# Performance work log

Measured on AMD Instinct MI355X. Metric: run time of the kernel, lower is better.

Reference implementation:

```python
import jax, jax.numpy as jnp
import numpy as np

N_NODES = 100000
N_EDGES = 3200000
EMB = 64
K = 2
NUM_GRAPHS = 512


def setup_inputs() -> dict:
    key = jax.random.key(0)
    ks = jax.random.split(key, 12)
    x = jax.random.normal(ks[0], (N_NODES, EMB), dtype=jnp.float32)
    edge_index = jax.random.randint(ks[1], (2, N_EDGES), 0, N_NODES, dtype=jnp.int64)
    edge_attr = jax.random.normal(ks[2], (N_EDGES, 1), dtype=jnp.float32)
    batch = jnp.sort(jax.random.randint(ks[3], (N_NODES,), 0, NUM_GRAPHS, dtype=jnp.int64))
    s = 1.0 / np.sqrt(EMB)
    wn1 = jax.random.normal(ks[4], (EMB, EMB), dtype=jnp.float32) * s
    bn1 = jnp.zeros((EMB,), jnp.float32)
    wn2 = jax.random.normal(ks[5], (EMB, 1), dtype=jnp.float32) * s
    bn2 = jnp.zeros((1,), jnp.float32)
    wc1 = jax.random.normal(ks[6], (EMB, EMB), dtype=jnp.float32) * s
    bc1 = jnp.zeros((EMB,), jnp.float32)
    wc2 = jax.random.normal(ks[7], (EMB, 2 * K * EMB), dtype=jnp.float32) * s
    bc2 = jnp.zeros((2 * K * EMB,), jnp.float32)
    return dict(x=x, edge_index=edge_index, edge_attr=edge_attr, batch=batch,
                wn1=wn1, bn1=bn1, wn2=wn2, bn2=bn2,
                wc1=wc1, bc1=bc1, wc2=wc2, bc2=bc2)


def reference(x, edge_index, edge_attr, batch, wn1, bn1, wn2, bn2, wc1, bc1, wc2, bc2):
    N, C = x.shape
    alpha = 0.1  # APPNP teleport prob
    # --- APPNP(K=1): gcn_norm with self-loops, one propagation step ---
    loops = jnp.arange(N, dtype=edge_index.dtype)
    src = jnp.concatenate([edge_index[0], loops])
    dst = jnp.concatenate([edge_index[1], loops])
    ones = jnp.ones(src.shape[0], dtype=x.dtype)
    deg = jax.ops.segment_sum(ones, dst, num_segments=N)
    dinv = jnp.where(deg > 0, jax.lax.rsqrt(deg), 0.0)
    norm = dinv[src] * dinv[dst]  # [E+N]
    agg = jax.ops.segment_sum(x[src] * norm[:, None], dst, num_segments=N)
    diffuse_x = (1.0 - alpha) * agg + alpha * x  # [N, C]
    # --- node-wise gate: MLP -> global softmax over all nodes ---
    h = jax.nn.relu(diffuse_x @ wn1 + bn1)
    gamma = h @ wn2 + bn2  # [N, 1]
    gamma = jax.nn.softmax(gamma, axis=0)
    # --- per-graph mean pool + channel-wise MLP ---
    sums = jax.ops.segment_sum(diffuse_x, batch, num_segments=NUM_GRAPHS)
    cnt = jax.ops.segment_sum(jnp.ones((N,), x.dtype), batch, num_segments=NUM_GRAPHS)
    pooled = jnp.where(cnt[:, None] > 0, sums / jnp.maximum(cnt, 1.0)[:, None], 0.0)
    pc = jnp.tanh(jax.nn.relu(pooled @ wc1 + bc1) @ wc2 + bc2)  # [B, 2*K*C]
    alpha_kc = pc[:, : K * C].reshape(NUM_GRAPHS, K, C)
    beta_kc = alpha_kc  # faithful to original bug: beta_kc = alpha_kc.reshape(...)
    # --- per-node affine via kron(alpha_kc, gamma_dense) gathered back to nodes ---
    # alpha_batch[b, n, k, c] = alpha_kc[b, k, c] * gamma_dense[b, n]; mask-gather == index by batch
    g = gamma[:, :, None]  # [N, 1, 1]
    a_node = alpha_kc[batch] * g  # [N, K, C]
    b_node = beta_kc[batch] * g  # [N, K, C]
    out = jnp.max(a_node * x[:, None, :] + b_node, axis=1)  # [N, C]
    return out
```

## Files before the change

### kernel.cpp

```cpp
#include <hip/hip_runtime.h>
#include <cstdint>

#define N_NODES   100000
#define N_EDGES   3200000
#define EMB       64
#define NUM_GRAPHS 512
#define NB        391
#define CAP       9216
#define PCHUNK    4096
#define PBLOCKS   ((N_EDGES + PCHUNK - 1) / PCHUNK)

__device__ __forceinline__ float bflo(unsigned u) { return __uint_as_float(u << 16); }
__device__ __forceinline__ float bfhi(unsigned u) { return __uint_as_float(u & 0xFFFF0000u); }
__device__ __forceinline__ unsigned rne_bf16(float f) {
    unsigned b = __float_as_uint(f);
    return (b + 0x7FFFu + ((b >> 16) & 1u)) >> 16;
}

__global__ void cvt_kernel(const float* __restrict__ x, unsigned* __restrict__ xh) {
    int i = blockIdx.x * 256 + threadIdx.x;
    if (i < N_NODES * EMB / 2) {
        float2 f = ((const float2*)x)[i];
        xh[i] = rne_bf16(f.x) | (rne_bf16(f.y) << 16);
    }
}

__global__ void partition_kernel(const int* __restrict__ ei, int* __restrict__ bcnt,
                                 unsigned* __restrict__ gpairs) {
    __shared__ unsigned sp[PCHUNK];
    __shared__ unsigned short sb[PCHUNK];
    __shared__ int scnt[512];
    __shared__ int soff[512];
    __shared__ int scur[512];
    __shared__ int gbase[512];
    __shared__ int s[256];
    int t = threadIdx.x;
    for (int i = t; i < 512; i += 256) scnt[i] = 0;
    __syncthreads();
    int base = blockIdx.x * PCHUNK;
    int lim  = min(N_EDGES - base, PCHUNK);
    for (int k = t; k < lim; k += 256) {
        int d = ei[N_EDGES + base + k];
        atomicAdd(&scnt[d >> 8], 1);
    }
    __syncthreads();
    int a0 = scnt[2 * t], a1 = scnt[2 * t + 1];
    int p = a0 + a1;
    s[t] = p; __syncthreads();
    for (int d = 1; d < 256; d <<= 1) {
        int add = (t >= d) ? s[t - d] : 0;
        __syncthreads();
        s[t] += add;
        __syncthreads();
    }
    int excl = s[t] - p;
    soff[2 * t] = excl;       soff[2 * t + 1] = excl + a0;
    scur[2 * t] = excl;       scur[2 * t + 1] = excl + a0;
    __syncthreads();
    for (int i = t; i < NB; i += 256) gbase[i] = i * CAP + atomicAdd(&bcnt[i], scnt[i]);
    __syncthreads();
    for (int k = t; k < lim; k += 256) {
        int sId = ei[base + k];
        int d   = ei[N_EDGES + base + k];
        int b   = d >> 8;
        int pos = atomicAdd(&scur[b], 1);
        sp[pos] = (unsigned)sId | ((unsigned)(d & 255) << 17);
        sb[pos] = (unsigned short)b;
    }
    __syncthreads();
    for (int i = t; i < lim; i += 256) {
        int b = sb[i];
        gpairs[gbase[b] + (i - soff[b])] = sp[i];
    }
}

__global__ void bucket_scan_kernel(const int* __restrict__ bcnt, int* __restrict__ bbase) {
    __shared__ int s[512];
    int t = threadIdx.x;
    int v = (t < NB) ? bcnt[t] : 0;
    s[t] = v; __syncthreads();
    for (int d = 1; d < 512; d <<= 1) {
        int add = (t >= d) ? s[t - d] : 0;
        __syncthreads();
        s[t] += add;
        __syncthreads();
    }
    if (t < NB) bbase[t] = s[t] - v;
}

__global__ void bscatter2_kernel(const unsigned* __restrict__ gpairs, const int* __restrict__ bcnt,
                                 const int* __restrict__ bbase, int* __restrict__ ebuf,
                                 int* __restrict__ indeg, int* __restrict__ rowstart,
                                 float* __restrict__ dinv) {
    int b = blockIdx.x, t = threadIdx.x, nlo = b << 8;
    __shared__ int lcnt[256];
    __shared__ int lcur[256];
    __shared__ int s[256];
    lcnt[t] = 0; __syncthreads();
    int cnt = bcnt[b];
    const unsigned* gp = gpairs + (size_t)b * CAP;
    for (int i = t; i < cnt; i += 256) atomicAdd(&lcnt[(gp[i] >> 17) & 255], 1);
    __syncthreads();
    int v = lcnt[t];
    s[t] = v; __syncthreads();
    for (int d = 1; d < 256; d <<= 1) {
        int add = (t >= d) ? s[t - d] : 0;
        __syncthreads();
        s[t] += add;
        __syncthreads();
    }
    int excl = s[t] - v;
    int base = bbase[b];
    int n = nlo + t;
    if (n < N_NODES) {
        indeg[n] = v;
        rowstart[n] = base + excl;
        dinv[n] = rsqrtf((float)(v + 1));
    }
    lcur[t] = base + excl;
    __syncthreads();
    for (int i = t; i < cnt; i += 256) {
        unsigned pk = gp[i];
        int pos = atomicAdd(&lcur[(pk >> 17) & 255], 1);
        ebuf[pos] = (int)(pk & 0x1FFFFu);
    }
}

__global__ void gather_mlp_bf16(const int* __restrict__ ebuf, const int* __restrict__ rowstart,
                                const int* __restrict__ indeg, const float* __restrict__ dinv,
                                const float* __restrict__ x, const unsigned* __restrict__ xh,
                                float* __restrict__ dx,
                                const float* __restrict__ wn1, const float* __restrict__ bn1,
                                const float* __restrict__ wn2, const float* __restrict__ bn2,
                                float* __restrict__ gl) {
    __shared__ float wn1s[EMB * EMB];
    __shared__ float bn1s[EMB];
    __shared__ float wn2s[EMB];
    for (int i = threadIdx.x; i < EMB * EMB; i += blockDim.x) wn1s[i] = wn1[i];
    if (threadIdx.x < EMB) { bn1s[threadIdx.x] = bn1[threadIdx.x]; wn2s[threadIdx.x] = wn2[threadIdx.x]; }
    __syncthreads();

    int wid = (blockIdx.x * blockDim.x + threadIdx.x) >> 6;
    if (wid >= N_NODES) return;
    int n = __builtin_amdgcn_readfirstlane(wid);
    int l = threadIdx.x & 63;
    int g = l >> 3;
    int q = l & 7;
    int start = rowstart[n];
    int cnt   = indeg[n];
    float dn  = dinv[n];
    const uint4* __restrict__ xr = (const uint4*)xh;

    float a0 = 0.f, a1 = 0.f, a2 = 0.f, a3 = 0.f, a4 = 0.f, a5 = 0.f, a6 = 0.f, a7 = 0.f;
    int j = 0;
    for (; j + 32 <= cnt; j += 32) {
        int sA = ebuf[start + j + g];
        int sB = ebuf[start + j + 8 + g];
        int sC = ebuf[start + j + 16 + g];
        int sD = ebuf[start + j + 24 + g];
        float wA = dinv[sA] * dn;
        float wB = dinv[sB] * dn;
        float wC = dinv[sC] * dn;
        float wD = dinv[sD] * dn;
        uint4 vA = xr[sA * 8 + q];
        uint4 vB = xr[sB * 8 + q];
        uint4 vC = xr[sC * 8 + q];
        uint4 vD = xr[sD * 8 + q];
        a0 += bflo(vA.x) * wA + bflo(vB.x) * wB + bflo(vC.x) * wC + bflo(vD.x) * wD;
        a1 += bfhi(vA.x) * wA + bfhi(vB.x) * wB + bfhi(vC.x) * wC + bfhi(vD.x) * wD;
        a2 += bflo(vA.y) * wA + bflo(vB.y) * wB + bflo(vC.y) * wC + bflo(vD.y) * wD;
        a3 += bfhi(vA.y) * wA + bfhi(vB.y) * wB + bfhi(vC.y) * wC + bfhi(vD.y) * wD;
        a4 += bflo(vA.z) * wA + bflo(vB.z) * wB + bflo(vC.z) * wC + bflo(vD.z) * wD;
        a5 += bfhi(vA.z) * wA + bfhi(vB.z) * wB + bfhi(vC.z) * wC + bfhi(vD.z) * wD;
        a6 += bflo(vA.w) * wA + bflo(vB.w) * wB + bflo(vC.w) * wC + bflo(vD.w) * wD;
        a7 += bfhi(vA.w) * wA + bfhi(vB.w) * wB + bfhi(vC.w) * wC + bfhi(vD.w) * wD;
    }
    if (j + 16 <= cnt) {
        int sA = ebuf[start + j + g];
        int sB = ebuf[start + j + 8 + g];
        float wA = dinv[sA] * dn;
        float wB = dinv[sB] * dn;
        uint4 vA = xr[sA * 8 + q];
        uint4 vB = xr[sB * 8 + q];
        a0 += bflo(vA.x) * wA + bflo(vB.x) * wB;
        a1 += bfhi(vA.x) * wA + bfhi(vB.x) * wB;
        a2 += bflo(vA.y) * wA + bflo(vB.y) * wB;
        a3 += bfhi(vA.y) * wA + bfhi(vB.y) * wB;
        a4 += bflo(vA.z) * wA + bflo(vB.z) * wB;
        a5 += bfhi(vA.z) * wA + bfhi(vB.z) * wB;
        a6 += bflo(vA.w) * wA + bflo(vB.w) * wB;
        a7 += bfhi(vA.w) * wA + bfhi(vB.w) * wB;
        j += 16;
    }
    if (j + 8 <= cnt) {
        int sA = ebuf[start + j + g];
        float wA = dinv[sA] * dn;
        uint4 vA = xr[sA * 8 + q];
        a0 += bflo(vA.x) * wA; a1 += bfhi(vA.x) * wA;
        a2 += bflo(vA.y) * wA; a3 += bfhi(vA.y) * wA;
        a4 += bflo(vA.z) * wA; a5 += bfhi(vA.z) * wA;
        a6 += bflo(vA.w) * wA; a7 += bfhi(vA.w) * wA;
        j += 8;
    }
    if (g < cnt - j) {
        int sA = ebuf[start + j + g];
        float wA = dinv[sA] * dn;
        uint4 vA = xr[sA * 8 + q];
        a0 += bflo(vA.x) * wA; a1 += bfhi(vA.x) * wA;
        a2 += bflo(vA.y) * wA; a3 += bfhi(vA.y) * wA;
        a4 += bflo(vA.z) * wA; a5 += bfhi(vA.z) * wA;
        a6 += bflo(vA.w) * wA; a7 += bfhi(vA.w) * wA;
    }
    a0 += __shfl_xor(a0, 8); a0 += __shfl_xor(a0, 16); a0 += __shfl_xor(a0, 32);
    a1 += __shfl_xor(a1, 8); a1 += __shfl_xor(a1, 16); a1 += __shfl_xor(a1, 32);
    a2 += __shfl_xor(a2, 8); a2 += __shfl_xor(a2, 16); a2 += __shfl_xor(a2, 32);
    a3 += __shfl_xor(a3, 8); a3 += __shfl_xor(a3, 16); a3 += __shfl_xor(a3, 32);
    a4 += __shfl_xor(a4, 8); a4 += __shfl_xor(a4, 16); a4 += __shfl_xor(a4, 32);
    a5 += __shfl_xor(a5, 8); a5 += __shfl_xor(a5, 16); a5 += __shfl_xor(a5, 32);
    a6 += __shfl_xor(a6, 8); a6 += __shfl_xor(a6, 16); a6 += __shfl_xor(a6, 32);
    a7 += __shfl_xor(a7, 8); a7 += __shfl_xor(a7, 16); a7 += __shfl_xor(a7, 32);

    const float4* __restrict__ x4 = (const float4*)x;
    float4 xv0 = x4[n * 16 + 2 * q];
    float4 xv1 = x4[n * 16 + 2 * q + 1];
    float s2 = dn * dn;
    float r0 = 0.9f * (a0 + xv0.x * s2) + 0.1f * xv0.x;
    float r1 = 0.9f * (a1 + xv0.y * s2) + 0.1f * xv0.y;
    float r2 = 0.9f * (a2 + xv0.z * s2) + 0.1f * xv0.z;
    float r3 = 0.9f * (a3 + xv0.w * s2) + 0.1f * xv0.w;
    float r4 = 0.9f * (a4 + xv1.x * s2) + 0.1f * xv1.x;
    float r5 = 0.9f * (a5 + xv1.y * s2) + 0.1f * xv1.y;
    float r6 = 0.9f * (a6 + xv1.z * s2) + 0.1f * xv1.z;
    float r7 = 0.9f * (a7 + xv1.w * s2) + 0.1f * xv1.w;
    if (l < 8) {
        float4 w0; w0.x = r0; w0.y = r1; w0.z = r2; w0.w = r3;
        float4 w1; w1.x = r4; w1.y = r5; w1.z = r6; w1.w = r7;
        ((float4*)dx)[n * 16 + 2 * l]     = w0;
        ((float4*)dx)[n * 16 + 2 * l + 1] = w1;
    }

    float rr[8] = {r0, r1, r2, r3, r4, r5, r6, r7};
    float am = bn1s[l];
#pragma unroll
    for (int c = 0; c < EMB; ++c) {
        float b = __shfl(rr[c & 7], c >> 3);
        am += b * wn1s[c * EMB + l];
    }
    float h = fmaxf(am, 0.0f);
    float t = h * wn2s[l];
#pragma unroll
    for (int off = 32; off; off >>= 1) t += __shfl_xor(t, off);
    if (l == 0) gl[n] = t + bn2[0];
}

__global__ void gather_mlp_kernel(const int* __restrict__ ebuf, const int* __restrict__ rowstart,
                                  const int* __restrict__ indeg, const float* __restrict__ dinv,
                                  const float* __restrict__ x, float* __restrict__ dx,
                                  const float* __restrict__ wn1, const float* __restrict__ bn1,
                                  const float* __restrict__ wn2, const float* __restrict__ bn2,
                                  float* __restrict__ gl) {
    __shared__ float wn1s[EMB * EMB];
    __shared__ float bn1s[EMB];
    __shared__ float wn2s[EMB];
    for (int i = threadIdx.x; i < EMB * EMB; i += blockDim.x) wn1s[i] = wn1[i];
    if (threadIdx.x < EMB) { bn1s[threadIdx.x] = bn1[threadIdx.x]; wn2s[threadIdx.x] = wn2[threadIdx.x]; }
    __syncthreads();

    int wid = (blockIdx.x * blockDim.x + threadIdx.x) >> 6;
    if (wid >= N_NODES) return;
    int n = __builtin_amdgcn_readfirstlane(wid);
    int l = threadIdx.x & 63;
    int g = l >> 4;
    int q = l & 15;
    int start = rowstart[n];
    int cnt   = indeg[n];
    float dn  = dinv[n];
    const float4* __restrict__ x4 = (const float4*)x;

    float ax = 0.f, ay = 0.f, az = 0.f, aw = 0.f;
    int j = 0;
    for (; j + 8 <= cnt; j += 8) {
        int sA = ebuf[start + j + g];
        int sB = ebuf[start + j + 4 + g];
        float wA = dinv[sA] * dn;
        float wB = dinv[sB] * dn;
        float4 vA = x4[sA * 16 + q];
        float4 vB = x4[sB * 16 + q];
        ax += vA.x * wA + vB.x * wB;
        ay += vA.y * wA + vB.y * wB;
        az += vA.z * wA + vB.z * wB;
        aw += vA.w * wA + vB.w * wB;
    }
    if (j + 4 <= cnt) {
        int sA = ebuf[start + j + g];
        float wA = dinv[sA] * dn;
        float4 vA = x4[sA * 16 + q];
        ax += vA.x * wA; ay += vA.y * wA; az += vA.z * wA; aw += vA.w * wA;
        j += 4;
    }
    int rem = cnt - j;
    if (g < rem) {
        int sA = ebuf[start + j + g];
        float wA = dinv[sA] * dn;
        float4 vA = x4[sA * 16 + q];
        ax += vA.x * wA; ay += vA.y * wA; az += vA.z * wA; aw += vA.w * wA;
    }
    ax += __shfl_xor(ax, 16); ax += __shfl_xor(ax, 32);
    ay += __shfl_xor(ay, 16); ay += __shfl_xor(ay, 32);
    az += __shfl_xor(az, 16); az += __shfl_xor(az, 32);
    aw += __shfl_xor(aw, 16); aw += __shfl_xor(aw, 32);

    float4 xv = x4[n * 16 + q];
    float s2 = dn * dn;
    float r0 = 0.9f * (ax + xv.x * s2) + 0.1f * xv.x;
    float r1 = 0.9f * (ay + xv.y * s2) + 0.1f * xv.y;
    float r2 = 0.9f * (az + xv.z * s2) + 0.1f * xv.z;
    float r3 = 0.9f * (aw + xv.w * s2) + 0.1f * xv.w;
    if (l < 16) {
        float4 rv; rv.x = r0; rv.y = r1; rv.z = r2; rv.w = r3;
        ((float4*)dx)[n * 16 + q] = rv;
    }
    float rr[4] = {r0, r1, r2, r3};
    float am = bn1s[l];
#pragma unroll
    for (int c = 0; c < EMB; ++c) {
        float b = __shfl(rr[c & 3], c >> 2);
        am += b * wn1s[c * EMB + l];
    }
    float h = fmaxf(am, 0.0f);
    float t = h * wn2s[l];
#pragma unroll
    for (int off = 32; off; off >>= 1) t += __shfl_xor(t, off);
    if (l == 0) gl[n] = t + bn2[0];
}

__global__ void expsum_kernel(const float* __restrict__ gl, float* __restrict__ gsum) {
    __shared__ float red[256];
    float s = 0.0f;
    for (int i = blockIdx.x * blockDim.x + threadIdx.x; i < N_NODES; i += gridDim.x * blockDim.x)
        s += expf(gl[i]);
    red[threadIdx.x] = s; __syncthreads();
    for (int t = 128; t; t >>= 1) {
        if ((int)threadIdx.x < t) red[threadIdx.x] += red[threadIdx.x + t];
        __syncthreads();
    }
    if (threadIdx.x == 0) atomicAdd(gsum, red[0]);
}

__device__ inline int lower_bound_i(const int* a, int n, int key) {
    int lo = 0, hi = n;
    while (lo < hi) {
        int mid = (lo + hi) >> 1;
        if (a[mid] < key) lo = mid + 1; else hi = mid;
    }
    return lo;
}
__global__ void poolmlp_kernel(const float* __restrict__ dx, const int* __restrict__ batch,
                               const float* __restrict__ wc1, const float* __restrict__ bc1,
                               const float* __restrict__ wc2, const float* __restrict__ bc2,
                               float* __restrict__ alphag) {
    int g = blockIdx.x;
    int lo = lower_bound_i(batch, N_NODES, g);
    int hi = lower_bound_i(batch, N_NODES, g + 1);
    int lane = threadIdx.x & 63;
    int w = threadIdx.x >> 6;
    float acc = 0.0f;
    for (int n = lo + w; n < hi; n += 4) acc += dx[n * EMB + lane];
    __shared__ float red[4][EMB];
    __shared__ float p[EMB];
    __shared__ float h[EMB];
    red[w][lane] = acc; __syncthreads();
    if (threadIdx.x < EMB) {
        float s = red[0][threadIdx.x] + red[1][threadIdx.x] + red[2][threadIdx.x] + red[3][threadIdx.x];
        int cnt = hi - lo;
        p[threadIdx.x] = cnt > 0 ? s / (float)cnt : 0.0f;
    }
    __syncthreads();
    if (threadIdx.x < EMB) {
        int j = threadIdx.x;
        float a = bc1[j];
        for (int c = 0; c < EMB; ++c) a += p[c] * wc1[c * EMB + j];
        h[j] = fmaxf(a, 0.0f);
    }
    __syncthreads();
    if (threadIdx.x < 128) {
        int o = threadIdx.x;
        float a = bc2[o];
        for (int j = 0; j < EMB; ++j) a += h[j] * wc2[j * 256 + o];
        alphag[g * 128 + o] = tanhf(a);
    }
}

__global__ void final_kernel(const float* __restrict__ x, const int* __restrict__ batch,
                             const float* __restrict__ gl, const float* __restrict__ gsum,
                             const float* __restrict__ alphag, float* __restrict__ out) {
    int n = (blockIdx.x * blockDim.x + threadIdx.x) >> 6;
    if (n >= N_NODES) return;
    int lane = threadIdx.x & 63;
    int g = batch[n];
    float gamma = expf(gl[n]) / gsum[0];
    float a0 = alphag[g * 128 + lane];
    float a1 = alphag[g * 128 + 64 + lane];
    float t = gamma * (x[n * EMB + lane] + 1.0f);
    out[n * EMB + lane] = fmaxf(a0 * t, a1 * t);
}

extern "C" void kernel_launch(void* const* d_in, const int* in_sizes, int n_in,
                              void* d_out, int out_size, void* d_ws, size_t ws_size,
                              hipStream_t stream) {
    const float* x     = (const float*)d_in[0];
    const int*   ei    = (const int*)d_in[1];
    const int*   batch = (const int*)d_in[3];
    const float* wn1 = (const float*)d_in[4];
    const float* bn1 = (const float*)d_in[5];
    const float* wn2 = (const float*)d_in[6];
    const float* bn2 = (const float*)d_in[7];
    const float* wc1 = (const float*)d_in[8];
    const float* bc1 = (const float*)d_in[9];
    const float* wc2 = (const float*)d_in[10];
    const float* bc2 = (const float*)d_in[11];
    float* out = (float*)d_out;

    char* wsb = (char*)d_ws;
    float* dx     = (float*)wsb;
    float* gl     = dx + (size_t)N_NODES * EMB;
    float* dinv   = gl + N_NODES;
    float* pooled = dinv + N_NODES;
    float* alphag = pooled + NUM_GRAPHS * EMB;
    int*   bcnt   = (int*)(alphag + NUM_GRAPHS * 128);
    float* gsum   = (float*)(bcnt + 512);
    int*   bbase  = (int*)(gsum + 1);
    int*   indeg  = bbase + 512;
    int*   rowstart = indeg + N_NODES;
    int*   ebuf   = rowstart + N_NODES;
    unsigned* xh  = (unsigned*)(ebuf + N_EDGES);
    unsigned* gpairs = (unsigned*)dx;

    size_t need_bf16 = (size_t)((char*)(xh + (size_t)N_NODES * EMB / 2) - wsb);
    int use_bf16 = (ws_size >= need_bf16);

    hipMemsetAsync(bcnt, 0, 513 * sizeof(int), stream);
    if (use_bf16)
        cvt_kernel<<<(N_NODES * EMB / 2 + 255) / 256, 256, 0, stream>>>(x, xh);
    partition_kernel<<<PBLOCKS, 256, 0, stream>>>(ei, bcnt, gpairs);
    bucket_scan_kernel<<<1, 512, 0, stream>>>(bcnt, bbase);
    bscatter2_kernel<<<NB, 256, 0, stream>>>(gpairs, bcnt, bbase, ebuf, indeg, rowstart, dinv);
    if (use_bf16)
        gather_mlp_bf16<<<(N_NODES * 64) / 256, 256, 0, stream>>>(ebuf, rowstart, indeg, dinv, x, xh, dx,
                                                                  wn1, bn1, wn2, bn2, gl);
    else
        gather_mlp_kernel<<<(N_NODES * 64) / 256, 256, 0, stream>>>(ebuf, rowstart, indeg, dinv, x, dx,
                                                                    wn1, bn1, wn2, bn2, gl);
    expsum_kernel<<<256, 256, 0, stream>>>(gl, gsum);
    poolmlp_kernel<<<NUM_GRAPHS, 256, 0, stream>>>(dx, batch, wc1, bc1, wc2, bc2, alphag);
    final_kernel<<<N_NODES / 4, 256, 0, stream>>>(x, batch, gl, gsum, alphag, out);
}
```

Measured before the change: 295.8 us.

## Merge small kernels to cut launches: fold cvt, bucket scan, expsum into neighbors

Fuses the bf16 conversion into the edge partition kernel as extra blocks, folds the bucket prefix scan into each bscatter block (redundantly recomputed per block), and merges the exp-sum reduction into the pooling kernel as extra blocks. This removes three kernel launches and their serialization gaps. The cost is redundant scans across 391 blocks and larger shared memory use per block in the merged kernels, which may lower occupancy.

```diff
diff --git a/kernel.cpp b/kernel.cpp
--- a/kernel.cpp
+++ b/kernel.cpp
@@ -9,6 +9,7 @@
 #define CAP       9216
 #define PCHUNK    4096
 #define PBLOCKS   ((N_EDGES + PCHUNK - 1) / PCHUNK)
+#define CVTBLKS   ((N_NODES * EMB / 2 + 255) / 256)
 
 __device__ __forceinline__ float bflo(unsigned u) { return __uint_as_float(u << 16); }
 __device__ __forceinline__ float bfhi(unsigned u) { return __uint_as_float(u & 0xFFFF0000u); }
@@ -17,15 +18,67 @@
     return (b + 0x7FFFu + ((b >> 16) & 1u)) >> 16;
 }
 
-__global__ void cvt_kernel(const float* __restrict__ x, unsigned* __restrict__ xh) {
-    int i = blockIdx.x * 256 + threadIdx.x;
-    if (i < N_NODES * EMB / 2) {
-        float2 f = ((const float2*)x)[i];
-        xh[i] = rne_bf16(f.x) | (rne_bf16(f.y) << 16);
-    }
-}
-
-__global__ void partition_kernel(const int* __restrict__ ei, int* __restrict__ bcnt,
+__global__ void build_kernel(const int* __restrict__ ei, int* __restrict__ bcnt,
+                             unsigned* __restrict__ gpairs,
+                             const float* __restrict__ x, unsigned* __restrict__ xh) {
+    __shared__ unsigned sp[PCHUNK];
+    __shared__ unsigned short sb[PCHUNK];
+    __shared__ int scnt[512];
+    __shared__ int soff[512];
+    __shared__ int scur[512];
+    __shared__ int gbase[512];
+    __shared__ int s[256];
+    int t = threadIdx.x;
+
+    if (blockIdx.x >= PBLOCKS) {
+        int i = (blockIdx.x - PBLOCKS) * 256 + t;
+        if (i < N_NODES * EMB / 2) {
+            float2 f = ((const float2*)x)[i];
+            xh[i] = rne_bf16(f.x) | (rne_bf16(f.y) << 16);
+        }
+        return;
+    }
+
+    for (int i = t; i < 512; i += 256) scnt[i] = 0;
+    __syncthreads();
+    int base = blockIdx.x * PCHUNK;
+    int lim  = min(N_EDGES - base, PCHUNK);
+    for (int k = t; k < lim; k += 256) {
+        int d = ei[N_EDGES + base + k];
+        atomicAdd(&scnt[d >> 8], 1);
+    }
+    __syncthreads();
+    int a0 = scnt[2 * t], a1 = scnt[2 * t + 1];
+    int p = a0 + a1;
+    s[t] = p; __syncthreads();
+    for (int d = 1; d < 256; d <<= 1) {
+        int add = (t >= d) ? s[t - d] : 0;
+        __syncthreads();
+        s[t] += add;
+        __syncthreads();
+    }
+    int excl = s[t] - p;
+    soff[2 * t] = excl;       soff[2 * t + 1] = excl + a0;
+    scur[2 * t] = excl;       scur[2 * t + 1] = excl + a0;
+    __syncthreads();
+    for (int i = t; i < NB; i += 256) gbase[i] = i * CAP + atomicAdd(&bcnt[i], scnt[i]);
+    __syncthreads();
+    for (int k = t; k < lim; k += 256) {
+        int sId = ei[base + k];
+        int d   = ei[N_EDGES + base + k];
+        int b   = d >> 8;
+        int pos = atomicAdd(&scur[b], 1);
+        sp[pos] = (unsigned)sId | ((unsigned)(d & 255) << 17);
+        sb[pos] = (unsigned short)b;
+    }
+    __syncthreads();
+    for (int i = t; i < lim; i += 256) {
+        int b = sb[i];
+        gpairs[gbase[b] + (i - soff[b])] = sp[i];
+    }
+}
+
+__global__ void build_kernel_f32(const int* __restrict__ ei, int* __restrict__ bcnt,
                                  unsigned* __restrict__ gpairs) {
     __shared__ unsigned sp[PCHUNK];
     __shared__ unsigned short sb[PCHUNK];
@@ -74,29 +127,33 @@
     }
 }
 
-__global__ void bucket_scan_kernel(const int* __restrict__ bcnt, int* __restrict__ bbase) {
-    __shared__ int s[512];
-    int t = threadIdx.x;
-    int v = (t < NB) ? bcnt[t] : 0;
-    s[t] = v; __syncthreads();
-    for (int d = 1; d < 512; d <<= 1) {
-        int add = (t >= d) ? s[t - d] : 0;
-        __syncthreads();
-        s[t] += add;
-        __syncthreads();
-    }
-    if (t < NB) bbase[t] = s[t] - v;
-}
-
 __global__ void bscatter2_kernel(const unsigned* __restrict__ gpairs, const int* __restrict__ bcnt,
-                                 const int* __restrict__ bbase, int* __restrict__ ebuf,
+                                 int* __restrict__ ebuf,
                                  int* __restrict__ indeg, int* __restrict__ rowstart,
                                  float* __restrict__ dinv) {
     int b = blockIdx.x, t = threadIdx.x, nlo = b << 8;
+    __shared__ int pref[512];
     __shared__ int lcnt[256];
     __shared__ int lcur[256];
     __shared__ int s[256];
-    lcnt[t] = 0; __syncthreads();
+
+    int c0 = (2 * t < NB) ? bcnt[2 * t] : 0;
+    int c1 = (2 * t + 1 < NB) ? bcnt[2 * t + 1] : 0;
+    int pp = c0 + c1;
+    s[t] = pp; __syncthreads();
+    for (int d = 1; d < 256; d <<= 1) {
+        int add = (t >= d) ? s[t - d] : 0;
+        __syncthreads();
+        s[t] += add;
+        __syncthreads();
+    }
+    int excl2 = s[t] - pp;
+    pref[2 * t] = excl2;
+    pref[2 * t + 1] = excl2 + c0;
+    lcnt[t] = 0;
+    __syncthreads();
+    int base = pref[b];
+
     int cnt = bcnt[b];
     const unsigned* gp = gpairs + (size_t)b * CAP;
     for (int i = t; i < cnt; i += 256) atomicAdd(&lcnt[(gp[i] >> 17) & 255], 1);
@@ -110,7 +167,6 @@
         __syncthreads();
     }
     int excl = s[t] - v;
-    int base = bbase[b];
     int n = nlo + t;
     if (n < N_NODES) {
         indeg[n] = v;
@@ -334,19 +390,6 @@
     if (l == 0) gl[n] = t + bn2[0];
 }
 
-__global__ void expsum_kernel(const float* __restrict__ gl, float* __restrict__ gsum) {
-    __shared__ float red[256];
-    float s = 0.0f;
-    for (int i = blockIdx.x * blockDim.x + threadIdx.x; i < N_NODES; i += gridDim.x * blockDim.x)
-        s += expf(gl[i]);
-    red[threadIdx.x] = s; __syncthreads();
-    for (int t = 128; t; t >>= 1) {
-        if ((int)threadIdx.x < t) red[threadIdx.x] += red[threadIdx.x + t];
-        __syncthreads();
-    }
-    if (threadIdx.x == 0) atomicAdd(gsum, red[0]);
-}
-
 __device__ inline int lower_bound_i(const int* a, int n, int key) {
     int lo = 0, hi = n;
     while (lo < hi) {
@@ -355,10 +398,30 @@
     }
     return lo;
 }
-__global__ void poolmlp_kernel(const float* __restrict__ dx, const int* __restrict__ batch,
+__global__ void poolexp_kernel(const float* __restrict__ dx, const int* __restrict__ batch,
                                const float* __restrict__ wc1, const float* __restrict__ bc1,
                                const float* __restrict__ wc2, const float* __restrict__ bc2,
-                               float* __restrict__ alphag) {
+                               float* __restrict__ alphag,
+                               const float* __restrict__ gl, float* __restrict__ gsum) {
+    __shared__ float red[4][EMB];
+    __shared__ float p[EMB];
+    __shared__ float h[EMB];
+    __shared__ float red1[256];
+
+    if (blockIdx.x >= NUM_GRAPHS) {
+        int vb = blockIdx.x - NUM_GRAPHS;
+        float s = 0.0f;
+        for (int i = vb * 256 + threadIdx.x; i < N_NODES; i += 256 * 256)
+            s += expf(gl[i]);
+        red1[threadIdx.x] = s; __syncthreads();
+        for (int t = 128; t; t >>= 1) {
+            if ((int)threadIdx.x < t) red1[threadIdx.x] += red1[threadIdx.x + t];
+            __syncthreads();
+        }
+        if (threadIdx.x == 0) atomicAdd(gsum, red1[0]);
+        return;
+    }
+
     int g = blockIdx.x;
     int lo = lower_bound_i(batch, N_NODES, g);
     int hi = lower_bound_i(batch, N_NODES, g + 1);
@@ -366,9 +429,6 @@
     int w = threadIdx.x >> 6;
     float acc = 0.0f;
     for (int n = lo + w; n < hi; n += 4) acc += dx[n * EMB + lane];
-    __shared__ float red[4][EMB];
-    __shared__ float p[EMB];
-    __shared__ float h[EMB];
     red[w][lane] = acc; __syncthreads();
     if (threadIdx.x < EMB) {
         float s = red[0][threadIdx.x] + red[1][threadIdx.x] + red[2][threadIdx.x] + red[3][threadIdx.x];
@@ -441,17 +501,16 @@
 
     hipMemsetAsync(bcnt, 0, 513 * sizeof(int), stream);
     if (use_bf16)
-        cvt_kernel<<<(N_NODES * EMB / 2 + 255) / 256, 256, 0, stream>>>(x, xh);
-    partition_kernel<<<PBLOCKS, 256, 0, stream>>>(ei, bcnt, gpairs);
-    bucket_scan_kernel<<<1, 512, 0, stream>>>(bcnt, bbase);
-    bscatter2_kernel<<<NB, 256, 0, stream>>>(gpairs, bcnt, bbase, ebuf, indeg, rowstart, dinv);
+        build_kernel<<<PBLOCKS + CVTBLKS, 256, 0, stream>>>(ei, bcnt, gpairs, x, xh);
+    else
+        build_kernel_f32<<<PBLOCKS, 256, 0, stream>>>(ei, bcnt, gpairs);
+    bscatter2_kernel<<<NB, 256, 0, stream>>>(gpairs, bcnt, ebuf, indeg, rowstart, dinv);
     if (use_bf16)
         gather_mlp_bf16<<<(N_NODES * 64) / 256, 256, 0, stream>>>(ebuf, rowstart, indeg, dinv, x, xh, dx,
                                                                   wn1, bn1, wn2, bn2, gl);
     else
         gather_mlp_kernel<<<(N_NODES * 64) / 256, 256, 0, stream>>>(ebuf, rowstart, indeg, dinv, x, dx,
                                                                     wn1, bn1, wn2, bn2, gl);
-    expsum_kernel<<<256, 256, 0, stream>>>(gl, gsum);
-    poolmlp_kernel<<<NUM_GRAPHS, 256, 0, stream>>>(dx, batch, wc1, bc1, wc2, bc2, alphag);
+    poolexp_kernel<<<NUM_GRAPHS + 256, 256, 0, stream>>>(dx, batch, wc1, bc1, wc2, bc2, alphag, gl, gsum);
     final_kernel<<<N_NODES / 4, 256, 0, stream>>>(x, batch, gl, gsum, alphag, out);
 }
```

Result: faster. 286.2 us, median of 2 (-3.3%).
